# Kernel tuning notes

Hardware: AMD Instinct MI355X
Metric: run time of the kernel (lower is better)

The kernel has to match this reference:

```python
import jax, jax.numpy as jnp
import numpy as np

DIM_X, DIM_Y, BATCH = 64, 64, 2


def setup_inputs() -> dict:
    key = jax.random.key(0)
    k1, k2, k3 = jax.random.split(key, 3)
    mean_in = jax.random.normal(k1, (BATCH, DIM_X, DIM_Y), dtype=jnp.float32)
    # std must be positive
    std_in = jax.random.uniform(k2, (BATCH, DIM_X, DIM_Y), dtype=jnp.float32, minval=0.1, maxval=1.0)
    # identity correlation matrix -> PSD covariance, valid sqrt/div downstream
    n = DIM_X * DIM_Y
    corr_in = jnp.broadcast_to(jnp.eye(n, dtype=jnp.float32), (BATCH, n, n))
    # kaiming_uniform_(a=sqrt(5)) on a (dx, dy) weight -> bound = 1/sqrt(dy)
    bound = 1.0 / np.sqrt(DIM_Y)
    weight = jax.random.uniform(k3, (DIM_X, DIM_Y), dtype=jnp.float32, minval=-bound, maxval=bound)
    return {"mean_in": mean_in, "std_in": std_in, "corr_in": corr_in, "weight": weight}


def reference(mean_in, std_in, corr_in, weight):
    B, dx, dy = mean_in.shape
    n = dx * dy
    # fft(fft(w, dim=0), dim=1) == 2D FFT
    wfft = jnp.fft.fft2(weight)  # (dx, dy) complex

    # covariance from std and corr: cov[b,i,j,k,l] = std[b,i,j] * corr[b,i,j,k,l] * std[b,k,l]
    corr = corr_in.reshape(B, dx, dy, dx, dy)
    cov = std_in[:, None, None, :, :] * corr * std_in[:, :, :, None, None]

    # mean path: circular 2D convolution via FFT
    mean_fft = jnp.fft.fft2(mean_in, axes=(1, 2))
    mean_out = jnp.real(jnp.fft.ifft2(wfft[None] * mean_fft, axes=(1, 2)))

    # covariance path: 4D FFT, broadcast multiply by wfft on both index pairs, 4D IFFT
    cov_f = jnp.fft.fftn(cov, axes=(1, 2, 3, 4))
    cov_f = wfft[None, None, None, :, :] * cov_f * wfft[None, :, :, None, None]
    cov_out = jnp.real(jnp.fft.ifftn(cov_f, axes=(1, 2, 3, 4)))
    cov_out = cov_out.reshape(B, n, n)

    # update_correlation: std = sqrt(diag(cov)); corr = cov / (std outer std)
    var = jnp.diagonal(cov_out, axis1=-2, axis2=-1)  # (B, n)
    std_out = jnp.sqrt(jnp.maximum(var, 1e-12))
    denom = std_out[:, :, None] * std_out[:, None, :]
    corr_out = cov_out / denom
    std_out = std_out.reshape(B, dx, dy)
    return mean_out, std_out, corr_out
```

## Files before the change

### kernel.cpp

```cpp
#include <hip/hip_runtime.h>
#include <math.h>

#define DXY   64
#define NN    4096
#define NB    2
#define CP    65

#define C16 0.9238795325112867f
#define S16 0.3826834323650898f
#define R22 0.7071067811865476f

__device__ __forceinline__ void cmul_ip(float2& a, float wr, float wi) {
    float t = a.x * wr - a.y * wi;
    a.y = a.x * wi + a.y * wr;
    a.x = t;
}

__device__ __forceinline__ void bf4(float2* y, int i0, int i1, int i2, int i3, int inv) {
    float2 a0 = y[i0], a1 = y[i1], a2 = y[i2], a3 = y[i3];
    float t0r = a0.x + a2.x, t0i = a0.y + a2.y;
    float t1r = a0.x - a2.x, t1i = a0.y - a2.y;
    float t2r = a1.x + a3.x, t2i = a1.y + a3.y;
    float dr  = a1.x - a3.x, di  = a1.y - a3.y;
    float t3r, t3i;
    if (inv) { t3r = -di; t3i = dr; } else { t3r = di; t3i = -dr; }
    y[i0] = make_float2(t0r + t2r, t0i + t2i);
    y[i1] = make_float2(t1r + t3r, t1i + t3i);
    y[i2] = make_float2(t0r - t2r, t0i - t2i);
    y[i3] = make_float2(t1r - t3r, t1i - t3i);
}

__device__ __forceinline__ void fft16_fwd(float2* y) {
    bf4(y, 0, 4, 8, 12, 0);
    bf4(y, 1, 5, 9, 13, 0);
    cmul_ip(y[5],  C16, -S16); cmul_ip(y[9],  R22, -R22); cmul_ip(y[13],  S16, -C16);
    bf4(y, 2, 6, 10, 14, 0);
    cmul_ip(y[6],  R22, -R22); cmul_ip(y[10], 0.f, -1.f); cmul_ip(y[14], -R22, -R22);
    bf4(y, 3, 7, 11, 15, 0);
    cmul_ip(y[7],  S16, -C16); cmul_ip(y[11], -R22, -R22); cmul_ip(y[15], -C16,  S16);
    bf4(y, 0, 1, 2, 3, 0); bf4(y, 4, 5, 6, 7, 0);
    bf4(y, 8, 9, 10, 11, 0); bf4(y, 12, 13, 14, 15, 0);
}

__device__ __forceinline__ void fft16_inv(float2* y) {
    bf4(y, 0, 1, 2, 3, 1); bf4(y, 4, 5, 6, 7, 1);
    bf4(y, 8, 9, 10, 11, 1); bf4(y, 12, 13, 14, 15, 1);
    cmul_ip(y[5],  C16,  S16); cmul_ip(y[9],  R22,  R22); cmul_ip(y[13],  S16,  C16);
    cmul_ip(y[6],  R22,  R22); cmul_ip(y[10], 0.f,  1.f); cmul_ip(y[14], -R22,  R22);
    cmul_ip(y[7],  S16,  C16); cmul_ip(y[11], -R22,  R22); cmul_ip(y[15], -C16, -S16);
    bf4(y, 0, 4, 8, 12, 1); bf4(y, 1, 5, 9, 13, 1);
    bf4(y, 2, 6, 10, 14, 1); bf4(y, 3, 7, 11, 15, 1);
}

template<int US, int NS, bool FUSEW>
__device__ void fwd_pass(float2* z, const float2* __restrict__ wf, int u, int k1,
                         float c1r, float c1i, float s2, float2 Wb)
{
    const int B = u * US;
    float2 y[16];
    float twr = 1.f, twi = 0.f;
#pragma unroll
    for (int n2 = 0; n2 < 16; ++n2) {
        float2 x0 = z[B + n2 * NS];
        float2 x1 = z[B + (n2 + 16) * NS];
        float2 x2 = z[B + (n2 + 32) * NS];
        float2 x3 = z[B + (n2 + 48) * NS];
        float er  = fmaf(s2, x2.x, x0.x), ei = fmaf(s2, x2.y, x0.y);
        float orr = fmaf(s2, x3.x, x1.x), oi = fmaf(s2, x3.y, x1.y);
        float br = er + c1r * orr - c1i * oi;
        float bi = ei + c1r * oi + c1i * orr;
        y[n2].x = twr * br - twi * bi;
        y[n2].y = twr * bi + twi * br;
        float t = twr * Wb.x - twi * Wb.y;
        twi = twr * Wb.y + twi * Wb.x;
        twr = t;
    }
    fft16_fwd(y);
    if (FUSEW) {
#pragma unroll
        for (int p = 0; p < 16; ++p) {
            float2 wv = wf[(16 * k1 + p) * 64 + u];
            cmul_ip(y[p], wv.x, wv.y);
        }
    }
    __syncthreads();
#pragma unroll
    for (int p = 0; p < 16; ++p) z[B + (16 * k1 + p) * NS] = y[p];
    __syncthreads();
}

template<int US, int NS>
__device__ void inv_pass(float2* z, int u, int k1,
                         float ci1r, float ci1i, float s2, float2 Wbc)
{
    const int B = u * US;
    float2 y[16];
#pragma unroll
    for (int p = 0; p < 16; ++p) y[p] = z[B + (16 * k1 + p) * NS];
    fft16_inv(y);
    float twr = 1.f, twi = 0.f;
#pragma unroll
    for (int n2 = 0; n2 < 16; ++n2) {
        cmul_ip(y[n2], twr, twi);
        float t = twr * Wbc.x - twi * Wbc.y;
        twi = twr * Wbc.y + twi * Wbc.x;
        twr = t;
    }
#pragma unroll
    for (int n2 = 0; n2 < 16; ++n2) z[B + (16 * k1 + n2) * NS] = y[n2];
    __syncthreads();
    float2 xx[16];
#pragma unroll
    for (int n2 = 0; n2 < 16; ++n2) {
        float2 h0 = z[B + n2 * NS];
        float2 h1 = z[B + (n2 + 16) * NS];
        float2 h2 = z[B + (n2 + 32) * NS];
        float2 h3 = z[B + (n2 + 48) * NS];
        float er  = fmaf(s2, h2.x, h0.x), ei = fmaf(s2, h2.y, h0.y);
        float orr = fmaf(s2, h3.x, h1.x), oi = fmaf(s2, h3.y, h1.y);
        xx[n2].x = er + ci1r * orr - ci1i * oi;
        xx[n2].y = ei + ci1r * oi + ci1i * orr;
    }
    __syncthreads();
#pragma unroll
    for (int n2 = 0; n2 < 16; ++n2) z[B + (16 * k1 + n2) * NS] = xx[n2];
    __syncthreads();
}

__global__ __launch_bounds__(256, 4)
void row_conv2_kernel(const float* __restrict__ in, float* __restrict__ out,
                      const float2* __restrict__ wfft_br,
                      const float* __restrict__ sstd,
                      const float* __restrict__ rstd,
                      const float* __restrict__ mean_i,
                      float* __restrict__ mean_o)
{
    __shared__ float2 z[64 * CP];
    const int tid = threadIdx.x;
    const int u   = ((tid >> 6) << 4) | (tid & 15);
    const int k1  = (tid >> 4) & 3;
    const float c1r = (k1 == 0) ? 1.f : ((k1 == 2) ? -1.f : 0.f);
    const float c1i = (k1 == 1) ? -1.f : ((k1 == 3) ? 1.f : 0.f);
    const float s2  = (k1 & 1) ? -1.f : 1.f;
    const float ang = -0.09817477042468103f * (float)k1;
    const float2 Wb  = make_float2(cosf(ang), sinf(ang));
    const float2 Wbc = make_float2(Wb.x, -Wb.y);
    const float ci1r = c1r, ci1i = -c1i;

    const float* ip = in;
    float*       op = out;
    const float* sstdp = sstd;
    const float* rstdp = rstd;
    int bid = blockIdx.x;
    if (mean_i && bid == (int)gridDim.x - 1) {
        ip = mean_i; op = mean_o; sstdp = nullptr; rstdp = nullptr; bid = 0;
    }

    const int row0 = 2 * bid;
    const long long off0 = (long long)row0 * NN, off1 = off0 + NN;
    const int b   = row0 >> 12;
    const int rI0 = row0 & (NN - 1), rI1 = rI0 + 1;
    const float* sb = nullptr;
    float sI0 = 1.f, sI1 = 1.f;
    if (sstdp) { sb = sstdp + (long long)b * NN; sI0 = sb[rI0]; sI1 = sb[rI1]; }

    float4 a4[4], c4[4], s4[4];
#pragma unroll
    for (int i = 0; i < 4; ++i) {
        int p = (tid + 256 * i) * 4;
        a4[i] = *(const float4*)(ip + off0 + p);
        c4[i] = *(const float4*)(ip + off1 + p);
    }
    if (sb) {
#pragma unroll
        for (int i = 0; i < 4; ++i) {
            int p = (tid + 256 * i) * 4;
            s4[i] = *(const float4*)(sb + p);
        }
    }
#pragma unroll
    for (int i = 0; i < 4; ++i) {
        int p = (tid + 256 * i) * 4;
        int r = p >> 6, c = p & 63;
        float4 a = a4[i], cc = c4[i];
        if (sb) {
            float4 s = s4[i];
            a.x *= sI0 * s.x; a.y *= sI0 * s.y; a.z *= sI0 * s.z; a.w *= sI0 * s.w;
            cc.x *= sI1 * s.x; cc.y *= sI1 * s.y; cc.z *= sI1 * s.z; cc.w *= sI1 * s.w;
        }
        float2* zp = z + r * CP + c;
        zp[0] = make_float2(a.x, cc.x);
        zp[1] = make_float2(a.y, cc.y);
        zp[2] = make_float2(a.z, cc.z);
        zp[3] = make_float2(a.w, cc.w);
    }
    __syncthreads();

    fwd_pass<CP, 1, false>(z, nullptr,  u, k1, c1r, c1i, s2, Wb);
    fwd_pass<1, CP, true >(z, wfft_br,  u, k1, c1r, c1i, s2, Wb);
    inv_pass<1, CP>(z, u, k1, ci1r, ci1i, s2, Wbc);
    inv_pass<CP, 1>(z, u, k1, ci1r, ci1i, s2, Wbc);

    const float scale = 1.0f / 4096.0f;
    float s0 = scale, s1 = scale;
    const float* rsb = nullptr;
    if (rstdp) {
        rsb = rstdp + (long long)b * NN;
        s0 *= rsb[rI0];
        s1 *= rsb[rI1];
    }
#pragma unroll
    for (int i = 0; i < 4; ++i) {
        int idx = tid + 256 * i;
        int p = idx * 4;
        int r = p >> 6, c = p & 63;
        const float2* zp = z + r * CP + c;
        float4 a, cc;
        a.x = zp[0].x; a.y = zp[1].x; a.z = zp[2].x; a.w = zp[3].x;
        cc.x = zp[0].y; cc.y = zp[1].y; cc.z = zp[2].y; cc.w = zp[3].y;
        if (rsb) {
            float4 rc = *(const float4*)(rsb + p);
            a.x *= s0 * rc.x; a.y *= s0 * rc.y; a.z *= s0 * rc.z; a.w *= s0 * rc.w;
            cc.x *= s1 * rc.x; cc.y *= s1 * rc.y; cc.z *= s1 * rc.z; cc.w *= s1 * rc.w;
        } else {
            a.x *= s0; a.y *= s0; a.z *= s0; a.w *= s0;
            cc.x *= s1; cc.y *= s1; cc.z *= s1; cc.w *= s1;
        }
        *(float4*)(op + off0 + p) = a;
        *(float4*)(op + off1 + p) = cc;
    }
}

__global__ __launch_bounds__(256, 4)
void wfft_kernel(const float* __restrict__ w, float2* wfft_br,
                 float* __restrict__ var_zero)
{
    __shared__ float2 z[64 * CP];
    const int tid = threadIdx.x;
#pragma unroll
    for (int i = 0; i < 32; ++i) var_zero[tid + 256 * i] = 0.f;
    const int u   = ((tid >> 6) << 4) | (tid & 15);
    const int k1  = (tid >> 4) & 3;
    const float c1r = (k1 == 0) ? 1.f : ((k1 == 2) ? -1.f : 0.f);
    const float c1i = (k1 == 1) ? -1.f : ((k1 == 3) ? 1.f : 0.f);
    const float s2  = (k1 & 1) ? -1.f : 1.f;
    const float ang = -0.09817477042468103f * (float)k1;
    const float2 Wb = make_float2(cosf(ang), sinf(ang));

#pragma unroll
    for (int i = 0; i < 16; ++i) {
        int p = tid + 256 * i;
        z[(p >> 6) * CP + (p & 63)] = make_float2(w[p], 0.f);
    }
    __syncthreads();
    fwd_pass<CP, 1, false>(z, nullptr, u, k1, c1r, c1i, s2, Wb);
    fwd_pass<1, CP, false>(z, nullptr, u, k1, c1r, c1i, s2, Wb);
#pragma unroll
    for (int i = 0; i < 16; ++i) {
        int p = tid + 256 * i;
        wfft_br[p] = z[(p >> 6) * CP + (p & 63)];
    }
}

__global__ __launch_bounds__(256, 4)
void transpose_inplace_kernel(float* data, const float* __restrict__ weight,
                              float* __restrict__ var)
{
    const int l = blockIdx.x;
    int bx = (int)((sqrtf(8.f * (float)l + 1.f) - 1.f) * 0.5f);
    while ((bx + 1) * (bx + 2) / 2 <= l) ++bx;
    while (bx * (bx + 1) / 2 > l) --bx;
    const int by = l - bx * (bx + 1) / 2;
    const int b  = blockIdx.y;

    __shared__ float tA[64 * 65];
    __shared__ float tB[64 * 65];
    __shared__ float wAs[64], wBs[64];
    __shared__ float red[512];
    const int tid = threadIdx.x;
    const int f  = tid & 15;
    const int r0 = tid >> 4;
    long long base = (long long)b * NN * NN;
    float* A  = data + base + (long long)(by * 64) * NN + bx * 64;
    float* Bt = data + base + (long long)(bx * 64) * NN + by * 64;

    if (tid < 64)       wAs[tid]      = weight[(((bx - by) & 63) << 6) + tid];
    else if (tid < 128) wBs[tid - 64] = weight[(((by - bx) & 63) << 6) + (tid - 64)];

    const int c = tid & 63, q = tid >> 6;

    if (bx == by) {
        float4 va[4];
#pragma unroll
        for (int it = 0; it < 4; ++it) {
            int r = r0 + 16 * it;
            va[it] = *(const float4*)(A + (long long)r * NN + 4 * f);
        }
#pragma unroll
        for (int it = 0; it < 4; ++it) {
            int r = r0 + 16 * it;
            tA[(4 * f + 0) * 65 + r] = va[it].x; tA[(4 * f + 1) * 65 + r] = va[it].y;
            tA[(4 * f + 2) * 65 + r] = va[it].z; tA[(4 * f + 3) * 65 + r] = va[it].w;
        }
        __syncthreads();
        float4 ov[4];
#pragma unroll
        for (int it = 0; it < 4; ++it) {
            int cc = r0 + 16 * it;
            ov[it].x = tA[cc * 65 + 4 * f + 0]; ov[it].y = tA[cc * 65 + 4 * f + 1];
            ov[it].z = tA[cc * 65 + 4 * f + 2]; ov[it].w = tA[cc * 65 + 4 * f + 3];
        }
        float sA = 0.f;
#pragma unroll
        for (int k = 0; k < 16; ++k) {
            int r = q * 16 + k;
            sA = fmaf(wAs[(c - r) & 63], tA[c * 65 + r], sA);
        }
        red[tid] = sA;
        __syncthreads();
        if (tid < 64) {
            float v = red[tid] + red[tid + 64] + red[tid + 128] + red[tid + 192];
            atomicAdd(&var[(long long)b * NN + bx * 64 + tid], v);
        }
#pragma unroll
        for (int it = 0; it < 4; ++it) {
            int cc = r0 + 16 * it;
            *(float4*)(A + (long long)cc * NN + 4 * f) = ov[it];
        }
    } else {
        float4 va[4], wb[4];
#pragma unroll
        for (int it = 0; it < 4; ++it) {
            int r = r0 + 16 * it;
            va[it] = *(const float4*)(A  + (long long)r * NN + 4 * f);
            wb[it] = *(const float4*)(Bt + (long long)r * NN + 4 * f);
        }
#pragma unroll
        for (int it = 0; it < 4; ++it) {
            int r = r0 + 16 * it;
            tA[(4 * f + 0) * 65 + r] = va[it].x; tA[(4 * f + 1) * 65 + r] = va[it].y;
            tA[(4 * f + 2) * 65 + r] = va[it].z; tA[(4 * f + 3) * 65 + r] = va[it].w;
            tB[(4 * f + 0) * 65 + r] = wb[it].x; tB[(4 * f + 1) * 65 + r] = wb[it].y;
            tB[(4 * f + 2) * 65 + r] = wb[it].z; tB[(4 * f + 3) * 65 + r] = wb[it].w;
        }
        __syncthreads();
        float4 ov[4], ow[4];
#pragma unroll
        for (int it = 0; it < 4; ++it) {
            int cc = r0 + 16 * it;
            ov[it].x = tB[cc * 65 + 4 * f + 0]; ov[it].y = tB[cc * 65 + 4 * f + 1];
            ov[it].z = tB[cc * 65 + 4 * f + 2]; ov[it].w = tB[cc * 65 + 4 * f + 3];
            ow[it].x = tA[cc * 65 + 4 * f + 0]; ow[it].y = tA[cc * 65 + 4 * f + 1];
            ow[it].z = tA[cc * 65 + 4 * f + 2]; ow[it].w = tA[cc * 65 + 4 * f + 3];
        }
        float sA = 0.f, sB = 0.f;
#pragma unroll
        for (int k = 0; k < 16; ++k) {
            int r = q * 16 + k;
            sA = fmaf(wAs[(c - r) & 63], tA[c * 65 + r], sA);
            sB = fmaf(wBs[(c - r) & 63], tB[c * 65 + r], sB);
        }
        red[tid] = sA; red[256 + tid] = sB;
        __syncthreads();
        if (tid < 64) {
            float v = red[tid] + red[tid + 64] + red[tid + 128] + red[tid + 192];
            atomicAdd(&var[(long long)b * NN + bx * 64 + tid], v);
        } else if (tid < 128) {
            int t = tid - 64;
            float v = red[256 + t] + red[320 + t] + red[384 + t] + red[448 + t];
            atomicAdd(&var[(long long)b * NN + by * 64 + t], v);
        }
#pragma unroll
        for (int it = 0; it < 4; ++it) {
            int cc = r0 + 16 * it;
            *(float4*)(A  + (long long)cc * NN + 4 * f) = ov[it];
            *(float4*)(Bt + (long long)cc * NN + 4 * f) = ow[it];
        }
    }
}

__global__ __launch_bounds__(256)
void std_kernel(const float* __restrict__ var, float* std_out, float* rstd, int n)
{
    int i = blockIdx.x * 256 + threadIdx.x;
    if (i < n) {
        float s = sqrtf(fmaxf(var[i], 1e-12f));
        std_out[i] = s;
        rstd[i] = 1.0f / s;
    }
}

extern "C" void kernel_launch(void* const* d_in, const int* in_sizes, int n_in,
                              void* d_out, int out_size, void* d_ws, size_t ws_size,
                              hipStream_t stream)
{
    const float* mean_in = (const float*)d_in[0];
    const float* std_in  = (const float*)d_in[1];
    const float* corr_in = (const float*)d_in[2];
    const float* weight  = (const float*)d_in[3];

    float* out      = (float*)d_out;
    float* mean_out = out;
    float* std_out  = out + 8192;
    float* corr_out = out + 16384;

    float*  ws      = (float*)d_ws;
    float2* wfft_br = (float2*)ws;
    float*  var_ws  = ws + 8192;
    float*  rstd_ws = ws + 16384;

    wfft_kernel<<<1, 256, 0, stream>>>(weight, wfft_br, var_ws);

    row_conv2_kernel<<<NB * NN / 2 + 1, 256, 0, stream>>>(
        corr_in, corr_out, wfft_br, std_in, nullptr, mean_in, mean_out);

    transpose_inplace_kernel<<<dim3(2080, NB), 256, 0, stream>>>(corr_out, weight,
                                                                 var_ws);

    std_kernel<<<(NB * NN + 255) / 256, 256, 0, stream>>>(var_ws, std_out,
                                                          rstd_ws, NB * NN);

    row_conv2_kernel<<<NB * NN / 2, 256, 0, stream>>>(
        corr_out, corr_out, wfft_br, nullptr, rstd_ws, nullptr, nullptr);
}
```

Before: 420.4 us.

## Make row FFT passes wave-local and fuse the column forward/inverse passes

Each 64-thread wavefront now loads and owns its own 16 rows of the 64x64 tile, so the row-direction FFT passes need no block-wide barrier. The forward column pass, the weight spectrum multiply and the inverse column pass are fused into one register-resident routine, which drops one shared-memory store/reload and several __syncthreads. The aim is to cut barrier stalls and LDS traffic in the FFT convolution kernel. In exchange it relies on intra-wavefront ordering of LDS accesses for correctness, and keeps more live registers in the fused column routine.

Measured after the change: 426.0 us. No clear change (+1.3%).

```diff
diff --git a/kernel.cpp b/kernel.cpp
--- a/kernel.cpp
+++ b/kernel.cpp
@@ -79,8 +79,8 @@
     if (FUSEW) {
 #pragma unroll
         for (int p = 0; p < 16; ++p) {
-            float2 wv = wf[(16 * k1 + p) * 64 + u];
-            cmul_ip(y[p], wv.x, wv.y);
+            float2 wv2 = wf[(16 * k1 + p) * 64 + u];
+            cmul_ip(y[p], wv2.x, wv2.y);
         }
     }
     __syncthreads();
@@ -89,16 +89,65 @@
     __syncthreads();
 }
 
-template<int US, int NS>
-__device__ void inv_pass(float2* z, int u, int k1,
-                         float ci1r, float ci1i, float s2, float2 Wbc)
-{
-    const int B = u * US;
+
+__device__ __forceinline__ void pass_fast_fwd(float2* z, int u, int k1,
+        float c1r, float c1i, float s2, float2 Wb)
+{
+    const int B = u * CP;
     float2 y[16];
-#pragma unroll
-    for (int p = 0; p < 16; ++p) y[p] = z[B + (16 * k1 + p) * NS];
+    float twr = 1.f, twi = 0.f;
+#pragma unroll
+    for (int n2 = 0; n2 < 16; ++n2) {
+        float2 x0 = z[B + n2];
+        float2 x1 = z[B + n2 + 16];
+        float2 x2 = z[B + n2 + 32];
+        float2 x3 = z[B + n2 + 48];
+        float er  = fmaf(s2, x2.x, x0.x), ei = fmaf(s2, x2.y, x0.y);
+        float orr = fmaf(s2, x3.x, x1.x), oi = fmaf(s2, x3.y, x1.y);
+        float br = er + c1r * orr - c1i * oi;
+        float bi = ei + c1r * oi + c1i * orr;
+        y[n2].x = twr * br - twi * bi;
+        y[n2].y = twr * bi + twi * br;
+        float t = twr * Wb.x - twi * Wb.y;
+        twi = twr * Wb.y + twi * Wb.x;
+        twr = t;
+    }
+    fft16_fwd(y);
+#pragma unroll
+    for (int p = 0; p < 16; ++p) z[B + 16 * k1 + p] = y[p];
+}
+
+__device__ __forceinline__ void pass_slow_fwd_inv(float2* z,
+        const float2* __restrict__ wf, int u, int k1,
+        float c1r, float c1i, float ci1r, float ci1i,
+        float s2, float2 Wb, float2 Wbc)
+{
+    float2 y[16];
+    float twr = 1.f, twi = 0.f;
+#pragma unroll
+    for (int n2 = 0; n2 < 16; ++n2) {
+        float2 x0 = z[u + n2 * CP];
+        float2 x1 = z[u + (n2 + 16) * CP];
+        float2 x2 = z[u + (n2 + 32) * CP];
+        float2 x3 = z[u + (n2 + 48) * CP];
+        float er  = fmaf(s2, x2.x, x0.x), ei = fmaf(s2, x2.y, x0.y);
+        float orr = fmaf(s2, x3.x, x1.x), oi = fmaf(s2, x3.y, x1.y);
+        float br = er + c1r * orr - c1i * oi;
+        float bi = ei + c1r * oi + c1i * orr;
+        y[n2].x = twr * br - twi * bi;
+        y[n2].y = twr * bi + twi * br;
+        float t = twr * Wb.x - twi * Wb.y;
+        twi = twr * Wb.y + twi * Wb.x;
+        twr = t;
+    }
+    fft16_fwd(y);
+#pragma unroll
+    for (int p = 0; p < 16; ++p) {
+        float2 wv2 = wf[(16 * k1 + p) * 64 + u];
+        cmul_ip(y[p], wv2.x, wv2.y);
+    }
     fft16_inv(y);
-    float twr = 1.f, twi = 0.f;
+    twr = 1.f; twi = 0.f;
 #pragma unroll
     for (int n2 = 0; n2 < 16; ++n2) {
         cmul_ip(y[n2], twr, twi);
@@ -107,24 +156,55 @@
         twr = t;
     }
 #pragma unroll
-    for (int n2 = 0; n2 < 16; ++n2) z[B + (16 * k1 + n2) * NS] = y[n2];
-    __syncthreads();
+    for (int n2 = 0; n2 < 16; ++n2) z[u + (16 * k1 + n2) * CP] = y[n2];
     float2 xx[16];
 #pragma unroll
     for (int n2 = 0; n2 < 16; ++n2) {
-        float2 h0 = z[B + n2 * NS];
-        float2 h1 = z[B + (n2 + 16) * NS];
-        float2 h2 = z[B + (n2 + 32) * NS];
-        float2 h3 = z[B + (n2 + 48) * NS];
+        float2 h0 = z[u + n2 * CP];
+        float2 h1 = z[u + (n2 + 16) * CP];
+        float2 h2 = z[u + (n2 + 32) * CP];
+        float2 h3 = z[u + (n2 + 48) * CP];
         float er  = fmaf(s2, h2.x, h0.x), ei = fmaf(s2, h2.y, h0.y);
         float orr = fmaf(s2, h3.x, h1.x), oi = fmaf(s2, h3.y, h1.y);
         xx[n2].x = er + ci1r * orr - ci1i * oi;
         xx[n2].y = ei + ci1r * oi + ci1i * orr;
     }
-    __syncthreads();
-#pragma unroll
-    for (int n2 = 0; n2 < 16; ++n2) z[B + (16 * k1 + n2) * NS] = xx[n2];
-    __syncthreads();
+#pragma unroll
+    for (int n2 = 0; n2 < 16; ++n2) z[u + (16 * k1 + n2) * CP] = xx[n2];
+}
+
+__device__ __forceinline__ void pass_fast_inv(float2* z, int u, int k1,
+        float ci1r, float ci1i, float s2, float2 Wbc)
+{
+    const int B = u * CP;
+    float2 y[16];
+#pragma unroll
+    for (int p = 0; p < 16; ++p) y[p] = z[B + 16 * k1 + p];
+    fft16_inv(y);
+    float twr = 1.f, twi = 0.f;
+#pragma unroll
+    for (int n2 = 0; n2 < 16; ++n2) {
+        cmul_ip(y[n2], twr, twi);
+        float t = twr * Wbc.x - twi * Wbc.y;
+        twi = twr * Wbc.y + twi * Wbc.x;
+        twr = t;
+    }
+#pragma unroll
+    for (int n2 = 0; n2 < 16; ++n2) z[B + 16 * k1 + n2] = y[n2];
+    float2 xx[16];
+#pragma unroll
+    for (int n2 = 0; n2 < 16; ++n2) {
+        float2 h0 = z[B + n2];
+        float2 h1 = z[B + n2 + 16];
+        float2 h2 = z[B + n2 + 32];
+        float2 h3 = z[B + n2 + 48];
+        float er  = fmaf(s2, h2.x, h0.x), ei = fmaf(s2, h2.y, h0.y);
+        float orr = fmaf(s2, h3.x, h1.x), oi = fmaf(s2, h3.y, h1.y);
+        xx[n2].x = er + ci1r * orr - ci1i * oi;
+        xx[n2].y = ei + ci1r * oi + ci1i * orr;
+    }
+#pragma unroll
+    for (int n2 = 0; n2 < 16; ++n2) z[B + 16 * k1 + n2] = xx[n2];
 }
 
 __global__ __launch_bounds__(256, 4)
@@ -139,6 +219,8 @@
     const int tid = threadIdx.x;
     const int u   = ((tid >> 6) << 4) | (tid & 15);
     const int k1  = (tid >> 4) & 3;
+    const int wv  = tid >> 6;
+    const int ln  = tid & 63;
     const float c1r = (k1 == 0) ? 1.f : ((k1 == 2) ? -1.f : 0.f);
     const float c1i = (k1 == 1) ? -1.f : ((k1 == 3) ? 1.f : 0.f);
     const float s2  = (k1 & 1) ? -1.f : 1.f;
@@ -167,20 +249,20 @@
     float4 a4[4], c4[4], s4[4];
 #pragma unroll
     for (int i = 0; i < 4; ++i) {
-        int p = (tid + 256 * i) * 4;
+        int p = 1024 * wv + 4 * ln + 256 * i;
         a4[i] = *(const float4*)(ip + off0 + p);
         c4[i] = *(const float4*)(ip + off1 + p);
     }
     if (sb) {
 #pragma unroll
         for (int i = 0; i < 4; ++i) {
-            int p = (tid + 256 * i) * 4;
+            int p = 1024 * wv + 4 * ln + 256 * i;
             s4[i] = *(const float4*)(sb + p);
         }
     }
 #pragma unroll
     for (int i = 0; i < 4; ++i) {
-        int p = (tid + 256 * i) * 4;
+        int p = 1024 * wv + 4 * ln + 256 * i;
         int r = p >> 6, c = p & 63;
         float4 a = a4[i], cc = c4[i];
         if (sb) {
@@ -194,12 +276,12 @@
         zp[2] = make_float2(a.z, cc.z);
         zp[3] = make_float2(a.w, cc.w);
     }
+
+    pass_fast_fwd(z, u, k1, c1r, c1i, s2, Wb);
     __syncthreads();
-
-    fwd_pass<CP, 1, false>(z, nullptr,  u, k1, c1r, c1i, s2, Wb);
-    fwd_pass<1, CP, true >(z, wfft_br,  u, k1, c1r, c1i, s2, Wb);
-    inv_pass<1, CP>(z, u, k1, ci1r, ci1i, s2, Wbc);
-    inv_pass<CP, 1>(z, u, k1, ci1r, ci1i, s2, Wbc);
+    pass_slow_fwd_inv(z, wfft_br, u, k1, c1r, c1i, ci1r, ci1i, s2, Wb, Wbc);
+    __syncthreads();
+    pass_fast_inv(z, u, k1, ci1r, ci1i, s2, Wbc);
 
     const float scale = 1.0f / 4096.0f;
     float s0 = scale, s1 = scale;
@@ -211,8 +293,7 @@
     }
 #pragma unroll
     for (int i = 0; i < 4; ++i) {
-        int idx = tid + 256 * i;
-        int p = idx * 4;
+        int p = 1024 * wv + 4 * ln + 256 * i;
         int r = p >> 6, c = p & 63;
         const float2* zp = z + r * CP + c;
         float4 a, cc;
```

## Switch row FFT to 8x8 decomposition with 512 threads and fused middle pass

Applied to the files above, without the earlier changes.

Restructures the 64-point FFT from a 4x16 split to an 8x8 split, so each thread handles 8 outputs and blocks grow to 512 threads. The second forward pass and first inverse pass are merged into one routine that keeps data in registers across the weight multiply, removing one shared-memory round trip and its barriers. The intent is more parallelism per row pair, lower register pressure per thread and less LDS traffic. In exchange, each output point of the cross stage now reads 8 inputs instead of 4.

After: 739.6 us. 75.9% more time.

```diff
diff --git a/kernel.cpp b/kernel.cpp
--- a/kernel.cpp
+++ b/kernel.cpp
@@ -6,8 +6,6 @@
 #define NB    2
 #define CP    65
 
-#define C16 0.9238795325112867f
-#define S16 0.3826834323650898f
 #define R22 0.7071067811865476f
 
 __device__ __forceinline__ void cmul_ip(float2& a, float wr, float wi) {
@@ -16,118 +14,183 @@
     a.x = t;
 }
 
-__device__ __forceinline__ void bf4(float2* y, int i0, int i1, int i2, int i3, int inv) {
-    float2 a0 = y[i0], a1 = y[i1], a2 = y[i2], a3 = y[i3];
-    float t0r = a0.x + a2.x, t0i = a0.y + a2.y;
-    float t1r = a0.x - a2.x, t1i = a0.y - a2.y;
-    float t2r = a1.x + a3.x, t2i = a1.y + a3.y;
-    float dr  = a1.x - a3.x, di  = a1.y - a3.y;
-    float t3r, t3i;
-    if (inv) { t3r = -di; t3i = dr; } else { t3r = di; t3i = -dr; }
-    y[i0] = make_float2(t0r + t2r, t0i + t2i);
-    y[i1] = make_float2(t1r + t3r, t1i + t3i);
-    y[i2] = make_float2(t0r - t2r, t0i - t2i);
-    y[i3] = make_float2(t1r - t3r, t1i - t3i);
-}
-
-__device__ __forceinline__ void fft16_fwd(float2* y) {
-    bf4(y, 0, 4, 8, 12, 0);
-    bf4(y, 1, 5, 9, 13, 0);
-    cmul_ip(y[5],  C16, -S16); cmul_ip(y[9],  R22, -R22); cmul_ip(y[13],  S16, -C16);
-    bf4(y, 2, 6, 10, 14, 0);
-    cmul_ip(y[6],  R22, -R22); cmul_ip(y[10], 0.f, -1.f); cmul_ip(y[14], -R22, -R22);
-    bf4(y, 3, 7, 11, 15, 0);
-    cmul_ip(y[7],  S16, -C16); cmul_ip(y[11], -R22, -R22); cmul_ip(y[15], -C16,  S16);
-    bf4(y, 0, 1, 2, 3, 0); bf4(y, 4, 5, 6, 7, 0);
-    bf4(y, 8, 9, 10, 11, 0); bf4(y, 12, 13, 14, 15, 0);
-}
-
-__device__ __forceinline__ void fft16_inv(float2* y) {
-    bf4(y, 0, 1, 2, 3, 1); bf4(y, 4, 5, 6, 7, 1);
-    bf4(y, 8, 9, 10, 11, 1); bf4(y, 12, 13, 14, 15, 1);
-    cmul_ip(y[5],  C16,  S16); cmul_ip(y[9],  R22,  R22); cmul_ip(y[13],  S16,  C16);
-    cmul_ip(y[6],  R22,  R22); cmul_ip(y[10], 0.f,  1.f); cmul_ip(y[14], -R22,  R22);
-    cmul_ip(y[7],  S16,  C16); cmul_ip(y[11], -R22,  R22); cmul_ip(y[15], -C16, -S16);
-    bf4(y, 0, 4, 8, 12, 1); bf4(y, 1, 5, 9, 13, 1);
-    bf4(y, 2, 6, 10, 14, 1); bf4(y, 3, 7, 11, 15, 1);
+__device__ __forceinline__ void bf2(float2& a, float2& b, float wr, float wi) {
+    float tr = a.x - b.x, ti = a.y - b.y;
+    a.x += b.x; a.y += b.y;
+    b.x = tr * wr - ti * wi;
+    b.y = tr * wi + ti * wr;
+}
+__device__ __forceinline__ void ibf2(float2& a, float2& b, float wr, float wi) {
+    float br = b.x * wr - b.y * wi, bi = b.x * wi + b.y * wr;
+    b.x = a.x - br; b.y = a.y - bi;
+    a.x += br; a.y += bi;
+}
+
+__device__ __forceinline__ void fft8_fwd(float2* y) {
+    bf2(y[0], y[4], 1.f, 0.f);  bf2(y[1], y[5],  R22, -R22);
+    bf2(y[2], y[6], 0.f, -1.f); bf2(y[3], y[7], -R22, -R22);
+    bf2(y[0], y[2], 1.f, 0.f);  bf2(y[1], y[3], 0.f, -1.f);
+    bf2(y[4], y[6], 1.f, 0.f);  bf2(y[5], y[7], 0.f, -1.f);
+    bf2(y[0], y[1], 1.f, 0.f);  bf2(y[2], y[3], 1.f, 0.f);
+    bf2(y[4], y[5], 1.f, 0.f);  bf2(y[6], y[7], 1.f, 0.f);
+}
+__device__ __forceinline__ void fft8_inv(float2* y) {
+    ibf2(y[0], y[1], 1.f, 0.f); ibf2(y[2], y[3], 1.f, 0.f);
+    ibf2(y[4], y[5], 1.f, 0.f); ibf2(y[6], y[7], 1.f, 0.f);
+    ibf2(y[0], y[2], 1.f, 0.f); ibf2(y[1], y[3], 0.f, 1.f);
+    ibf2(y[4], y[6], 1.f, 0.f); ibf2(y[5], y[7], 0.f, 1.f);
+    ibf2(y[0], y[4], 1.f, 0.f); ibf2(y[1], y[5],  R22,  R22);
+    ibf2(y[2], y[6], 0.f, 1.f); ibf2(y[3], y[7], -R22,  R22);
+}
+
+__device__ __forceinline__ float2 cross8(
+    float2 x0, float2 x1, float2 x2, float2 x3,
+    float2 x4, float2 x5, float2 x6, float2 x7,
+    float s2, float c1r, float c1i, float w8x, float w8y)
+{
+    float e0r = fmaf(s2, x4.x, x0.x), e0i = fmaf(s2, x4.y, x0.y);
+    float e1r = fmaf(s2, x5.x, x1.x), e1i = fmaf(s2, x5.y, x1.y);
+    float e2r = fmaf(s2, x6.x, x2.x), e2i = fmaf(s2, x6.y, x2.y);
+    float e3r = fmaf(s2, x7.x, x3.x), e3i = fmaf(s2, x7.y, x3.y);
+    float f0r = e0r + c1r * e2r - c1i * e2i;
+    float f0i = e0i + c1r * e2i + c1i * e2r;
+    float f1r = e1r + c1r * e3r - c1i * e3i;
+    float f1i = e1i + c1r * e3i + c1i * e3r;
+    float2 o;
+    o.x = f0r + w8x * f1r - w8y * f1i;
+    o.y = f0i + w8x * f1i + w8y * f1r;
+    return o;
 }
 
 template<int US, int NS, bool FUSEW>
-__device__ void fwd_pass(float2* z, const float2* __restrict__ wf, int u, int k1,
-                         float c1r, float c1i, float s2, float2 Wb)
+__device__ void fwd_pass8(float2* z, const float2* __restrict__ wf, int u, int k1,
+                          float c1r, float c1i, float s2,
+                          float w8x, float w8y, float2 Wb)
 {
     const int B = u * US;
-    float2 y[16];
+    float2 y[8];
     float twr = 1.f, twi = 0.f;
 #pragma unroll
-    for (int n2 = 0; n2 < 16; ++n2) {
-        float2 x0 = z[B + n2 * NS];
-        float2 x1 = z[B + (n2 + 16) * NS];
-        float2 x2 = z[B + (n2 + 32) * NS];
-        float2 x3 = z[B + (n2 + 48) * NS];
-        float er  = fmaf(s2, x2.x, x0.x), ei = fmaf(s2, x2.y, x0.y);
-        float orr = fmaf(s2, x3.x, x1.x), oi = fmaf(s2, x3.y, x1.y);
-        float br = er + c1r * orr - c1i * oi;
-        float bi = ei + c1r * oi + c1i * orr;
-        y[n2].x = twr * br - twi * bi;
-        y[n2].y = twr * bi + twi * br;
+    for (int n2 = 0; n2 < 8; ++n2) {
+        float2 b = cross8(z[B + n2 * NS],        z[B + (n2 +  8) * NS],
+                          z[B + (n2 + 16) * NS], z[B + (n2 + 24) * NS],
+                          z[B + (n2 + 32) * NS], z[B + (n2 + 40) * NS],
+                          z[B + (n2 + 48) * NS], z[B + (n2 + 56) * NS],
+                          s2, c1r, c1i, w8x, w8y);
+        y[n2].x = twr * b.x - twi * b.y;
+        y[n2].y = twr * b.y + twi * b.x;
         float t = twr * Wb.x - twi * Wb.y;
         twi = twr * Wb.y + twi * Wb.x;
         twr = t;
     }
-    fft16_fwd(y);
+    fft8_fwd(y);
     if (FUSEW) {
 #pragma unroll
-        for (int p = 0; p < 16; ++p) {
-            float2 wv = wf[(16 * k1 + p) * 64 + u];
+        for (int p = 0; p < 8; ++p) {
+            float2 wv = wf[(8 * k1 + p) * 64 + u];
             cmul_ip(y[p], wv.x, wv.y);
         }
     }
     __syncthreads();
 #pragma unroll
-    for (int p = 0; p < 16; ++p) z[B + (16 * k1 + p) * NS] = y[p];
+    for (int p = 0; p < 8; ++p) z[B + (8 * k1 + p) * NS] = y[p];
     __syncthreads();
 }
 
 template<int US, int NS>
-__device__ void inv_pass(float2* z, int u, int k1,
-                         float ci1r, float ci1i, float s2, float2 Wbc)
+__device__ void inv_pass8(float2* z, int u, int k1,
+                          float c1r, float c1i, float s2,
+                          float w8x, float w8y, float2 Wbc)
 {
     const int B = u * US;
-    float2 y[16];
-#pragma unroll
-    for (int p = 0; p < 16; ++p) y[p] = z[B + (16 * k1 + p) * NS];
-    fft16_inv(y);
+    float2 y[8];
+#pragma unroll
+    for (int p = 0; p < 8; ++p) y[p] = z[B + (8 * k1 + p) * NS];
+    fft8_inv(y);
     float twr = 1.f, twi = 0.f;
 #pragma unroll
-    for (int n2 = 0; n2 < 16; ++n2) {
+    for (int n2 = 0; n2 < 8; ++n2) {
         cmul_ip(y[n2], twr, twi);
         float t = twr * Wbc.x - twi * Wbc.y;
         twi = twr * Wbc.y + twi * Wbc.x;
         twr = t;
     }
 #pragma unroll
-    for (int n2 = 0; n2 < 16; ++n2) z[B + (16 * k1 + n2) * NS] = y[n2];
-    __syncthreads();
-    float2 xx[16];
-#pragma unroll
-    for (int n2 = 0; n2 < 16; ++n2) {
-        float2 h0 = z[B + n2 * NS];
-        float2 h1 = z[B + (n2 + 16) * NS];
-        float2 h2 = z[B + (n2 + 32) * NS];
-        float2 h3 = z[B + (n2 + 48) * NS];
-        float er  = fmaf(s2, h2.x, h0.x), ei = fmaf(s2, h2.y, h0.y);
-        float orr = fmaf(s2, h3.x, h1.x), oi = fmaf(s2, h3.y, h1.y);
-        xx[n2].x = er + ci1r * orr - ci1i * oi;
-        xx[n2].y = ei + ci1r * oi + ci1i * orr;
-    }
-    __syncthreads();
-#pragma unroll
-    for (int n2 = 0; n2 < 16; ++n2) z[B + (16 * k1 + n2) * NS] = xx[n2];
-    __syncthreads();
-}
-
-__global__ __launch_bounds__(256, 4)
+    for (int n2 = 0; n2 < 8; ++n2) z[B + (8 * k1 + n2) * NS] = y[n2];
+    __syncthreads();
+    float2 xx[8];
+#pragma unroll
+    for (int n2 = 0; n2 < 8; ++n2) {
+        xx[n2] = cross8(z[B + n2 * NS],        z[B + (n2 +  8) * NS],
+                        z[B + (n2 + 16) * NS], z[B + (n2 + 24) * NS],
+                        z[B + (n2 + 32) * NS], z[B + (n2 + 40) * NS],
+                        z[B + (n2 + 48) * NS], z[B + (n2 + 56) * NS],
+                        s2, c1r, c1i, w8x, w8y);
+    }
+    __syncthreads();
+#pragma unroll
+    for (int n2 = 0; n2 < 8; ++n2) z[B + (8 * k1 + n2) * NS] = xx[n2];
+    __syncthreads();
+}
+
+__device__ __forceinline__ void pass_slow8(float2* z, const float2* __restrict__ wf,
+        int u, int k1, float c1r, float c1i, float ci1r, float ci1i, float s2,
+        float w8x, float w8y, float w8cx, float w8cy, float2 Wb, float2 Wbc)
+{
+    float2 y[8];
+    {
+        float twr = 1.f, twi = 0.f;
+#pragma unroll
+        for (int n2 = 0; n2 < 8; ++n2) {
+            float2 b = cross8(z[u + n2 * CP],        z[u + (n2 +  8) * CP],
+                              z[u + (n2 + 16) * CP], z[u + (n2 + 24) * CP],
+                              z[u + (n2 + 32) * CP], z[u + (n2 + 40) * CP],
+                              z[u + (n2 + 48) * CP], z[u + (n2 + 56) * CP],
+                              s2, c1r, c1i, w8x, w8y);
+            y[n2].x = twr * b.x - twi * b.y;
+            y[n2].y = twr * b.y + twi * b.x;
+            float t = twr * Wb.x - twi * Wb.y;
+            twi = twr * Wb.y + twi * Wb.x;
+            twr = t;
+        }
+    }
+    fft8_fwd(y);
+#pragma unroll
+    for (int p = 0; p < 8; ++p) {
+        float2 wv = wf[(8 * k1 + p) * 64 + u];
+        cmul_ip(y[p], wv.x, wv.y);
+    }
+    fft8_inv(y);
+    {
+        float twr = 1.f, twi = 0.f;
+#pragma unroll
+        for (int n2 = 0; n2 < 8; ++n2) {
+            cmul_ip(y[n2], twr, twi);
+            float t = twr * Wbc.x - twi * Wbc.y;
+            twi = twr * Wbc.y + twi * Wbc.x;
+            twr = t;
+        }
+    }
+    __syncthreads();
+#pragma unroll
+    for (int n2 = 0; n2 < 8; ++n2) z[u + (8 * k1 + n2) * CP] = y[n2];
+    __syncthreads();
+    float2 xx[8];
+#pragma unroll
+    for (int n2 = 0; n2 < 8; ++n2) {
+        xx[n2] = cross8(z[u + n2 * CP],        z[u + (n2 +  8) * CP],
+                        z[u + (n2 + 16) * CP], z[u + (n2 + 24) * CP],
+                        z[u + (n2 + 32) * CP], z[u + (n2 + 40) * CP],
+                        z[u + (n2 + 48) * CP], z[u + (n2 + 56) * CP],
+                        s2, ci1r, ci1i, w8cx, w8cy);
+    }
+    __syncthreads();
+#pragma unroll
+    for (int n2 = 0; n2 < 8; ++n2) z[u + (8 * k1 + n2) * CP] = xx[n2];
+    __syncthreads();
+}
+
+__global__ __launch_bounds__(512, 8)
 void row_conv2_kernel(const float* __restrict__ in, float* __restrict__ out,
                       const float2* __restrict__ wfft_br,
                       const float* __restrict__ sstd,
@@ -137,15 +200,19 @@
 {
     __shared__ float2 z[64 * CP];
     const int tid = threadIdx.x;
-    const int u   = ((tid >> 6) << 4) | (tid & 15);
-    const int k1  = (tid >> 4) & 3;
-    const float c1r = (k1 == 0) ? 1.f : ((k1 == 2) ? -1.f : 0.f);
-    const float c1i = (k1 == 1) ? -1.f : ((k1 == 3) ? 1.f : 0.f);
+    const int u   = ((tid >> 6) << 3) | (tid & 7);
+    const int k1  = (tid >> 3) & 7;
+    const int k14 = k1 & 3;
+    const float c1r = (k14 == 0) ? 1.f : ((k14 == 2) ? -1.f : 0.f);
+    const float c1i = (k14 == 1) ? -1.f : ((k14 == 3) ? 1.f : 0.f);
     const float s2  = (k1 & 1) ? -1.f : 1.f;
+    const float a8  = -0.7853981633974483f * (float)k1;
+    const float w8x = cosf(a8), w8y = sinf(a8);
     const float ang = -0.09817477042468103f * (float)k1;
     const float2 Wb  = make_float2(cosf(ang), sinf(ang));
     const float2 Wbc = make_float2(Wb.x, -Wb.y);
     const float ci1r = c1r, ci1i = -c1i;
+    const float w8cx = w8x, w8cy = -w8y;
 
     const float* ip = in;
     float*       op = out;
@@ -164,23 +231,23 @@
     float sI0 = 1.f, sI1 = 1.f;
     if (sstdp) { sb = sstdp + (long long)b * NN; sI0 = sb[rI0]; sI1 = sb[rI1]; }
 
-    float4 a4[4], c4[4], s4[4];
-#pragma unroll
-    for (int i = 0; i < 4; ++i) {
-        int p = (tid + 256 * i) * 4;
+    float4 a4[2], c4[2], s4[2];
+#pragma unroll
+    for (int i = 0; i < 2; ++i) {
+        int p = (tid + 512 * i) * 4;
         a4[i] = *(const float4*)(ip + off0 + p);
         c4[i] = *(const float4*)(ip + off1 + p);
     }
     if (sb) {
 #pragma unroll
-        for (int i = 0; i < 4; ++i) {
-            int p = (tid + 256 * i) * 4;
+        for (int i = 0; i < 2; ++i) {
+            int p = (tid + 512 * i) * 4;
             s4[i] = *(const float4*)(sb + p);
         }
     }
 #pragma unroll
-    for (int i = 0; i < 4; ++i) {
-        int p = (tid + 256 * i) * 4;
+    for (int i = 0; i < 2; ++i) {
+        int p = (tid + 512 * i) * 4;
         int r = p >> 6, c = p & 63;
         float4 a = a4[i], cc = c4[i];
         if (sb) {
@@ -196,10 +263,10 @@
     }
     __syncthreads();
 
-    fwd_pass<CP, 1, false>(z, nullptr,  u, k1, c1r, c1i, s2, Wb);
-    fwd_pass<1, CP, true >(z, wfft_br,  u, k1, c1r, c1i, s2, Wb);
-    inv_pass<1, CP>(z, u, k1, ci1r, ci1i, s2, Wbc);
-    inv_pass<CP, 1>(z, u, k1, ci1r, ci1i, s2, Wbc);
+    fwd_pass8<CP, 1, false>(z, nullptr, u, k1, c1r, c1i, s2, w8x, w8y, Wb);
+    pass_slow8(z, wfft_br, u, k1, c1r, c1i, ci1r, ci1i, s2,
+               w8x, w8y, w8cx, w8cy, Wb, Wbc);
+    inv_pass8<CP, 1>(z, u, k1, ci1r, ci1i, s2, w8cx, w8cy, Wbc);
 
     const float scale = 1.0f / 4096.0f;
     float s0 = scale, s1 = scale;
@@ -210,9 +277,8 @@
         s1 *= rsb[rI1];
     }
 #pragma unroll
-    for (int i = 0; i < 4; ++i) {
-        int idx = tid + 256 * i;
-        int p = idx * 4;
+    for (int i = 0; i < 2; ++i) {
+        int p = (tid + 512 * i) * 4;
         int r = p >> 6, c = p & 63;
         const float2* zp = z + r * CP + c;
         float4 a, cc;
@@ -231,33 +297,36 @@
     }
 }
 
-__global__ __launch_bounds__(256, 4)
+__global__ __launch_bounds__(512, 8)
 void wfft_kernel(const float* __restrict__ w, float2* wfft_br,
                  float* __restrict__ var_zero)
 {
     __shared__ float2 z[64 * CP];
     const int tid = threadIdx.x;
 #pragma unroll
-    for (int i = 0; i < 32; ++i) var_zero[tid + 256 * i] = 0.f;
-    const int u   = ((tid >> 6) << 4) | (tid & 15);
-    const int k1  = (tid >> 4) & 3;
-    const float c1r = (k1 == 0) ? 1.f : ((k1 == 2) ? -1.f : 0.f);
-    const float c1i = (k1 == 1) ? -1.f : ((k1 == 3) ? 1.f : 0.f);
+    for (int i = 0; i < 16; ++i) var_zero[tid + 512 * i] = 0.f;
+    const int u   = ((tid >> 6) << 3) | (tid & 7);
+    const int k1  = (tid >> 3) & 7;
+    const int k14 = k1 & 3;
+    const float c1r = (k14 == 0) ? 1.f : ((k14 == 2) ? -1.f : 0.f);
+    const float c1i = (k14 == 1) ? -1.f : ((k14 == 3) ? 1.f : 0.f);
     const float s2  = (k1 & 1) ? -1.f : 1.f;
+    const float a8  = -0.7853981633974483f * (float)k1;
+    const float w8x = cosf(a8), w8y = sinf(a8);
     const float ang = -0.09817477042468103f * (float)k1;
     const float2 Wb = make_float2(cosf(ang), sinf(ang));
 
 #pragma unroll
-    for (int i = 0; i < 16; ++i) {
-        int p = tid + 256 * i;
+    for (int i = 0; i < 8; ++i) {
+        int p = tid + 512 * i;
         z[(p >> 6) * CP + (p & 63)] = make_float2(w[p], 0.f);
     }
     __syncthreads();
-    fwd_pass<CP, 1, false>(z, nullptr, u, k1, c1r, c1i, s2, Wb);
-    fwd_pass<1, CP, false>(z, nullptr, u, k1, c1r, c1i, s2, Wb);
-#pragma unroll
-    for (int i = 0; i < 16; ++i) {
-        int p = tid + 256 * i;
+    fwd_pass8<CP, 1, false>(z, nullptr, u, k1, c1r, c1i, s2, w8x, w8y, Wb);
+    fwd_pass8<1, CP, false>(z, nullptr, u, k1, c1r, c1i, s2, w8x, w8y, Wb);
+#pragma unroll
+    for (int i = 0; i < 8; ++i) {
+        int p = tid + 512 * i;
         wfft_br[p] = z[(p >> 6) * CP + (p & 63)];
     }
 }
@@ -409,9 +478,9 @@
     float*  var_ws  = ws + 8192;
     float*  rstd_ws = ws + 16384;
 
-    wfft_kernel<<<1, 256, 0, stream>>>(weight, wfft_br, var_ws);
-
-    row_conv2_kernel<<<NB * NN / 2 + 1, 256, 0, stream>>>(
+    wfft_kernel<<<1, 512, 0, stream>>>(weight, wfft_br, var_ws);
+
+    row_conv2_kernel<<<NB * NN / 2 + 1, 512, 0, stream>>>(
         corr_in, corr_out, wfft_br, std_in, nullptr, mean_in, mean_out);
 
     transpose_inplace_kernel<<<dim3(2080, NB), 256, 0, stream>>>(corr_out, weight,
@@ -420,6 +489,6 @@
     std_kernel<<<(NB * NN + 255) / 256, 256, 0, stream>>>(var_ws, std_out,
                                                           rstd_ws, NB * NN);
 
-    row_conv2_kernel<<<NB * NN / 2, 256, 0, stream>>>(
+    row_conv2_kernel<<<NB * NN / 2, 512, 0, stream>>>(
         corr_out, corr_out, wfft_br, nullptr, rstd_ws, nullptr, nullptr);
 }
```

## Widen LDS row pitch to 66 and use float4 LDS accesses in FFT passes

Applied to the files above, without the earlier changes.

Changes the shared-memory row padding from 65 to 66 complex elements so rows are 16-byte aligned. The FFT passes are restructured so the contiguous-axis gathers and stores use float4 (two complex values) LDS accesses instead of scalar float2 ones. The wfft kernel now writes its transposed output straight from registers rather than going through a second LDS pass. Even padding may bring back bank conflicts on the strided column accesses, which could cancel the gain from wider accesses.

New measurement: 452.8 us. 7.7% more time.

```diff
diff --git a/kernel.cpp b/kernel.cpp
--- a/kernel.cpp
+++ b/kernel.cpp
@@ -4,7 +4,7 @@
 #define DXY   64
 #define NN    4096
 #define NB    2
-#define CP    65
+#define CP    66
 
 #define C16 0.9238795325112867f
 #define S16 0.3826834323650898f
@@ -52,78 +52,153 @@
     bf4(y, 2, 6, 10, 14, 1); bf4(y, 3, 7, 11, 15, 1);
 }
 
-template<int US, int NS, bool FUSEW>
-__device__ void fwd_pass(float2* z, const float2* __restrict__ wf, int u, int k1,
-                         float c1r, float c1i, float s2, float2 Wb)
-{
-    const int B = u * US;
+__device__ __forceinline__ void gather_cross4(const float4* lp, float2* y,
+        float c1r, float c1i, float s2, float2 Wb)
+{
+    float twr = 1.f, twi = 0.f;
+#pragma unroll
+    for (int m = 0; m < 8; ++m) {
+        float4 A = lp[m];
+        float4 B = lp[m + 8];
+        float4 C = lp[m + 16];
+        float4 D = lp[m + 24];
+        {
+            float er  = fmaf(s2, C.x, A.x), ei = fmaf(s2, C.y, A.y);
+            float orr = fmaf(s2, D.x, B.x), oi = fmaf(s2, D.y, B.y);
+            float br = er + c1r * orr - c1i * oi;
+            float bi = ei + c1r * oi + c1i * orr;
+            y[2*m].x = twr * br - twi * bi;
+            y[2*m].y = twr * bi + twi * br;
+            float t = twr * Wb.x - twi * Wb.y;
+            twi = twr * Wb.y + twi * Wb.x; twr = t;
+        }
+        {
+            float er  = fmaf(s2, C.z, A.z), ei = fmaf(s2, C.w, A.w);
+            float orr = fmaf(s2, D.z, B.z), oi = fmaf(s2, D.w, B.w);
+            float br = er + c1r * orr - c1i * oi;
+            float bi = ei + c1r * oi + c1i * orr;
+            y[2*m+1].x = twr * br - twi * bi;
+            y[2*m+1].y = twr * bi + twi * br;
+            float t = twr * Wb.x - twi * Wb.y;
+            twi = twr * Wb.y + twi * Wb.x; twr = t;
+        }
+    }
+}
+
+__device__ __forceinline__ void gather_cross4_notw(const float4* lp, float2* xx,
+        float c1r, float c1i, float s2)
+{
+#pragma unroll
+    for (int m = 0; m < 8; ++m) {
+        float4 A = lp[m];
+        float4 B = lp[m + 8];
+        float4 C = lp[m + 16];
+        float4 D = lp[m + 24];
+        {
+            float er  = fmaf(s2, C.x, A.x), ei = fmaf(s2, C.y, A.y);
+            float orr = fmaf(s2, D.x, B.x), oi = fmaf(s2, D.y, B.y);
+            xx[2*m].x = er + c1r * orr - c1i * oi;
+            xx[2*m].y = ei + c1r * oi + c1i * orr;
+        }
+        {
+            float er  = fmaf(s2, C.z, A.z), ei = fmaf(s2, C.w, A.w);
+            float orr = fmaf(s2, D.z, B.z), oi = fmaf(s2, D.w, B.w);
+            xx[2*m+1].x = er + c1r * orr - c1i * oi;
+            xx[2*m+1].y = ei + c1r * oi + c1i * orr;
+        }
+    }
+}
+
+
+__device__ void p1_fast_fwd(float2* z, int u, int k1,
+        float c1r, float c1i, float s2, float2 Wb)
+{
     float2 y[16];
-    float twr = 1.f, twi = 0.f;
-#pragma unroll
-    for (int n2 = 0; n2 < 16; ++n2) {
-        float2 x0 = z[B + n2 * NS];
-        float2 x1 = z[B + (n2 + 16) * NS];
-        float2 x2 = z[B + (n2 + 32) * NS];
-        float2 x3 = z[B + (n2 + 48) * NS];
-        float er  = fmaf(s2, x2.x, x0.x), ei = fmaf(s2, x2.y, x0.y);
-        float orr = fmaf(s2, x3.x, x1.x), oi = fmaf(s2, x3.y, x1.y);
-        float br = er + c1r * orr - c1i * oi;
-        float bi = ei + c1r * oi + c1i * orr;
-        y[n2].x = twr * br - twi * bi;
-        y[n2].y = twr * bi + twi * br;
-        float t = twr * Wb.x - twi * Wb.y;
-        twi = twr * Wb.y + twi * Wb.x;
-        twr = t;
-    }
+    gather_cross4((const float4*)(z + u * CP), y, c1r, c1i, s2, Wb);
     fft16_fwd(y);
-    if (FUSEW) {
-#pragma unroll
-        for (int p = 0; p < 16; ++p) {
-            float2 wv = wf[(16 * k1 + p) * 64 + u];
-            cmul_ip(y[p], wv.x, wv.y);
-        }
-    }
-    __syncthreads();
-#pragma unroll
-    for (int p = 0; p < 16; ++p) z[B + (16 * k1 + p) * NS] = y[p];
-    __syncthreads();
-}
-
-template<int US, int NS>
-__device__ void inv_pass(float2* z, int u, int k1,
-                         float ci1r, float ci1i, float s2, float2 Wbc)
-{
-    const int B = u * US;
+    __syncthreads();
+#pragma unroll
+    for (int p = 0; p < 16; ++p) z[(16*k1 + p) * CP + u] = y[p];
+    __syncthreads();
+}
+
+__device__ void p2_slow_fwd(float2* z, const float2* __restrict__ wf, int u, int k1,
+        float c1r, float c1i, float s2, float2 Wb)
+{
     float2 y[16];
-#pragma unroll
-    for (int p = 0; p < 16; ++p) y[p] = z[B + (16 * k1 + p) * NS];
+    gather_cross4((const float4*)(z + u * CP), y, c1r, c1i, s2, Wb);
+    fft16_fwd(y);
+#pragma unroll
+    for (int p = 0; p < 16; ++p) {
+        float2 wv = wf[(16*k1 + p) * 64 + u];
+        cmul_ip(y[p], wv.x, wv.y);
+    }
+    __syncthreads();
+    float4* slot = (float4*)(z + u * CP + 16 * k1);
+#pragma unroll
+    for (int j = 0; j < 8; ++j)
+        slot[j] = make_float4(y[2*j].x, y[2*j].y, y[2*j+1].x, y[2*j+1].y);
+    __syncthreads();
+}
+
+__device__ void p3_slow_inv(float2* z, int u, int k1,
+        float ci1r, float ci1i, float s2, float2 Wbc)
+{
+    float2 y[16];
+    float4* slot = (float4*)(z + u * CP + 16 * k1);
+#pragma unroll
+    for (int j = 0; j < 8; ++j) {
+        float4 v = slot[j];
+        y[2*j]   = make_float2(v.x, v.y);
+        y[2*j+1] = make_float2(v.z, v.w);
+    }
     fft16_inv(y);
     float twr = 1.f, twi = 0.f;
 #pragma unroll
     for (int n2 = 0; n2 < 16; ++n2) {
         cmul_ip(y[n2], twr, twi);
         float t = twr * Wbc.x - twi * Wbc.y;
-        twi = twr * Wbc.y + twi * Wbc.x;
-        twr = t;
-    }
-#pragma unroll
-    for (int n2 = 0; n2 < 16; ++n2) z[B + (16 * k1 + n2) * NS] = y[n2];
+        twi = twr * Wbc.y + twi * Wbc.x; twr = t;
+    }
+#pragma unroll
+    for (int j = 0; j < 8; ++j)
+        slot[j] = make_float4(y[2*j].x, y[2*j].y, y[2*j+1].x, y[2*j+1].y);
     __syncthreads();
     float2 xx[16];
+    gather_cross4_notw((const float4*)(z + u * CP), xx, ci1r, ci1i, s2);
+    __syncthreads();
+#pragma unroll
+    for (int j = 0; j < 8; ++j)
+        slot[j] = make_float4(xx[2*j].x, xx[2*j].y, xx[2*j+1].x, xx[2*j+1].y);
+    __syncthreads();
+}
+
+__device__ void p4_fast_inv(float2* z, int u, int k1,
+        float ci1r, float ci1i, float s2, float2 Wbc)
+{
+    float2 y[16];
+#pragma unroll
+    for (int p = 0; p < 16; ++p) y[p] = z[(16*k1 + p) * CP + u];
+    fft16_inv(y);
+    float twr = 1.f, twi = 0.f;
 #pragma unroll
     for (int n2 = 0; n2 < 16; ++n2) {
-        float2 h0 = z[B + n2 * NS];
-        float2 h1 = z[B + (n2 + 16) * NS];
-        float2 h2 = z[B + (n2 + 32) * NS];
-        float2 h3 = z[B + (n2 + 48) * NS];
-        float er  = fmaf(s2, h2.x, h0.x), ei = fmaf(s2, h2.y, h0.y);
-        float orr = fmaf(s2, h3.x, h1.x), oi = fmaf(s2, h3.y, h1.y);
-        xx[n2].x = er + ci1r * orr - ci1i * oi;
-        xx[n2].y = ei + ci1r * oi + ci1i * orr;
-    }
-    __syncthreads();
-#pragma unroll
-    for (int n2 = 0; n2 < 16; ++n2) z[B + (16 * k1 + n2) * NS] = xx[n2];
+        cmul_ip(y[n2], twr, twi);
+        float t = twr * Wbc.x - twi * Wbc.y;
+        twi = twr * Wbc.y + twi * Wbc.x; twr = t;
+    }
+    __syncthreads();
+    float4* slot = (float4*)(z + u * CP + 16 * k1);
+#pragma unroll
+    for (int j = 0; j < 8; ++j)
+        slot[j] = make_float4(y[2*j].x, y[2*j].y, y[2*j+1].x, y[2*j+1].y);
+    __syncthreads();
+    float2 xx[16];
+    gather_cross4_notw((const float4*)(z + u * CP), xx, ci1r, ci1i, s2);
+    __syncthreads();
+#pragma unroll
+    for (int j = 0; j < 8; ++j)
+        slot[j] = make_float4(xx[2*j].x, xx[2*j].y, xx[2*j+1].x, xx[2*j+1].y);
     __syncthreads();
 }
 
@@ -188,18 +263,16 @@
             a.x *= sI0 * s.x; a.y *= sI0 * s.y; a.z *= sI0 * s.z; a.w *= sI0 * s.w;
             cc.x *= sI1 * s.x; cc.y *= sI1 * s.y; cc.z *= sI1 * s.z; cc.w *= sI1 * s.w;
         }
-        float2* zp = z + r * CP + c;
-        zp[0] = make_float2(a.x, cc.x);
-        zp[1] = make_float2(a.y, cc.y);
-        zp[2] = make_float2(a.z, cc.z);
-        zp[3] = make_float2(a.w, cc.w);
-    }
-    __syncthreads();
-
-    fwd_pass<CP, 1, false>(z, nullptr,  u, k1, c1r, c1i, s2, Wb);
-    fwd_pass<1, CP, true >(z, wfft_br,  u, k1, c1r, c1i, s2, Wb);
-    inv_pass<1, CP>(z, u, k1, ci1r, ci1i, s2, Wbc);
-    inv_pass<CP, 1>(z, u, k1, ci1r, ci1i, s2, Wbc);
+        float4* zp = (float4*)(z + r * CP + c);
+        zp[0] = make_float4(a.x, cc.x, a.y, cc.y);
+        zp[1] = make_float4(a.z, cc.z, a.w, cc.w);
+    }
+    __syncthreads();
+
+    p1_fast_fwd(z, u, k1, c1r, c1i, s2, Wb);
+    p2_slow_fwd(z, wfft_br, u, k1, c1r, c1i, s2, Wb);
+    p3_slow_inv(z, u, k1, ci1r, ci1i, s2, Wbc);
+    p4_fast_inv(z, u, k1, ci1r, ci1i, s2, Wbc);
 
     const float scale = 1.0f / 4096.0f;
     float s0 = scale, s1 = scale;
@@ -211,13 +284,12 @@
     }
 #pragma unroll
     for (int i = 0; i < 4; ++i) {
-        int idx = tid + 256 * i;
-        int p = idx * 4;
+        int p = (tid + 256 * i) * 4;
         int r = p >> 6, c = p & 63;
-        const float2* zp = z + r * CP + c;
-        float4 a, cc;
-        a.x = zp[0].x; a.y = zp[1].x; a.z = zp[2].x; a.w = zp[3].x;
-        cc.x = zp[0].y; cc.y = zp[1].y; cc.z = zp[2].y; cc.w = zp[3].y;
+        const float4* zp = (const float4*)(z + r * CP + c);
+        float4 v0 = zp[0], v1 = zp[1];
+        float4 a  = make_float4(v0.x, v0.z, v1.x, v1.z);
+        float4 cc = make_float4(v0.y, v0.w, v1.y, v1.w);
         if (rsb) {
             float4 rc = *(const float4*)(rsb + p);
             a.x *= s0 * rc.x; a.y *= s0 * rc.y; a.z *= s0 * rc.z; a.w *= s0 * rc.w;
@@ -253,13 +325,13 @@
         z[(p >> 6) * CP + (p & 63)] = make_float2(w[p], 0.f);
     }
     __syncthreads();
-    fwd_pass<CP, 1, false>(z, nullptr, u, k1, c1r, c1i, s2, Wb);
-    fwd_pass<1, CP, false>(z, nullptr, u, k1, c1r, c1i, s2, Wb);
-#pragma unroll
-    for (int i = 0; i < 16; ++i) {
-        int p = tid + 256 * i;
-        wfft_br[p] = z[(p >> 6) * CP + (p & 63)];
-    }
+    p1_fast_fwd(z, u, k1, c1r, c1i, s2, Wb);
+    float2 y[16];
+    gather_cross4((const float4*)(z + u * CP), y, c1r, c1i, s2, Wb);
+    fft16_fwd(y);
+#pragma unroll
+    for (int p = 0; p < 16; ++p)
+        wfft_br[(16 * k1 + p) * 64 + u] = y[p];
 }
 
 __global__ __launch_bounds__(256, 4)
```
